# Kernel optimization log

Hardware: AMD Instinct MI355X
Metric: run time of the kernel (lower is better)

## Reference

```python
import jax, jax.numpy as jnp
import numpy as np

DIM = 3072
NUM_HEADS = 24
HEAD_DIM = DIM // NUM_HEADS  # 128
EPS = 1e-6


def rms_norm(x, scale):
    # x: (..., D); torch F.rms_norm over last dim
    var = jnp.mean(jnp.square(x), axis=-1, keepdims=True)
    return x * jax.lax.rsqrt(var + EPS) * scale


def apply_rope(xq, xk, freqs_cis):
    # xq, xk: (B, H, L, D); freqs_cis: (1, 1, L, D//2, 2, 2)
    B, H, L, D = xq.shape
    xq_ = xq.astype(jnp.float32).reshape(B, H, L, D // 2, 1, 2)
    xk_ = xk.astype(jnp.float32).reshape(B, H, L, D // 2, 1, 2)
    # (1,1,L,D/2,2) * (B,H,L,D/2,1) broadcast -> (B,H,L,D/2,2)
    xq_out = freqs_cis[..., 0] * xq_[..., 0] + freqs_cis[..., 1] * xq_[..., 1]
    xk_out = freqs_cis[..., 0] * xk_[..., 0] + freqs_cis[..., 1] * xk_[..., 1]
    return xq_out.reshape(B, H, L, D).astype(xq.dtype), xk_out.reshape(B, H, L, D).astype(xk.dtype)


def setup_inputs() -> dict:
    key = jax.random.key(0)
    ks = jax.random.split(key, 7)
    B, L = 1, 2048
    x = jax.random.normal(ks[0], (B, L, DIM), dtype=jnp.float32)
    pe = jax.random.normal(ks[1], (1, 1, L, HEAD_DIM // 2, 2, 2), dtype=jnp.float32)
    # parameters (torch nn.Linear layout: weight is (out, in))
    s = 1.0 / np.sqrt(DIM)
    w_qkv = jax.random.uniform(ks[2], (3 * DIM, DIM), minval=-s, maxval=s, dtype=jnp.float32)
    w_proj = jax.random.uniform(ks[3], (DIM, DIM), minval=-s, maxval=s, dtype=jnp.float32)
    b_proj = jax.random.uniform(ks[4], (DIM,), minval=-s, maxval=s, dtype=jnp.float32)
    q_scale = jnp.ones((HEAD_DIM,), dtype=jnp.float32)
    k_scale = jnp.ones((HEAD_DIM,), dtype=jnp.float32)
    return {"x": x, "pe": pe, "w_qkv": w_qkv, "w_proj": w_proj,
            "b_proj": b_proj, "q_scale": q_scale, "k_scale": k_scale}


def reference(x, pe, w_qkv, w_proj, b_proj, q_scale, k_scale):
    B, L, _ = x.shape
    qkv = x @ w_qkv.T  # (B, L, 3*DIM)
    qkv = qkv.reshape(B, L, 3, NUM_HEADS, HEAD_DIM)
    qkv = jnp.transpose(qkv, (2, 0, 3, 1, 4))  # (3, B, H, L, D)
    q, k, v = qkv[0], qkv[1], qkv[2]
    # QKNorm (RMSNorm over head_dim)
    q = rms_norm(q, q_scale)
    k = rms_norm(k, k_scale)
    # RoPE
    q, k = apply_rope(q, k, pe)
    # SDPA: softmax(q k^T / sqrt(D)) v, non-causal
    scores = jnp.einsum("bhqd,bhkd->bhqk", q, k) / np.sqrt(HEAD_DIM).astype(np.float32)
    attn = jax.nn.softmax(scores, axis=-1)
    out = jnp.einsum("bhqk,bhkd->bhqd", attn, v)  # (B, H, L, D)
    out = jnp.transpose(out, (0, 2, 1, 3)).reshape(B, L, DIM)  # B L (H D)
    return out @ w_proj.T + b_proj
```

## Files before the change

### kernel.cpp

```cpp
#include <hip/hip_runtime.h>
#include <hip/hip_bf16.h>

typedef _Float16 f16;
typedef _Float16 f16x2 __attribute__((ext_vector_type(2)));
typedef _Float16 f16x4 __attribute__((ext_vector_type(4)));
typedef _Float16 f16x8 __attribute__((ext_vector_type(8)));
typedef float f32x4 __attribute__((ext_vector_type(4)));

#define L_SEQ 2048
#define DIM 3072
#define NHEAD 24
#define HDIM 128

__device__ __forceinline__ void gll16(const f16* g, f16* l) {
    __builtin_amdgcn_global_load_lds((const __attribute__((address_space(1))) void*)g,
                                     (__attribute__((address_space(3))) void*)l, 16, 0, 0);
}

__global__ __launch_bounds__(256) void f32_to_f16_kernel(const float* __restrict__ s,
                                                         f16* __restrict__ d, int n4) {
    int i = blockIdx.x * blockDim.x + threadIdx.x;
    int stride = gridDim.x * blockDim.x;
    for (; i < n4; i += stride) {
        float4 v = reinterpret_cast<const float4*>(s)[i];
        f16x4 o = {(f16)v.x, (f16)v.y, (f16)v.z, (f16)v.w};
        reinterpret_cast<f16x4*>(d)[i] = o;
    }
}


#define PH_BODY(T, VM, DO_STAGE)                                                        \
    {                                                                                   \
        const int slot_ = (T) % 3;                                                      \
        const int s2_ = ((T) + 2) % 3;                                                  \
        const f16* Asl = &As[slot_][0];                                                 \
        const f16* Bsl = &Bs[slot_][0];                                                 \
                        \
        asm volatile("s_waitcnt vmcnt(" #VM ")" ::: "memory");                          \
        __builtin_amdgcn_s_barrier();                                                   \
        __builtin_amdgcn_sched_barrier(0);                                              \
                             \
        f16x8 bf[4][2], af[2][2];                                                       \
        _Pragma("unroll") for (int j = 0; j < 4; j++)                                   \
            _Pragma("unroll") for (int kk = 0; kk < 2; kk++)                            \
                bf[j][kk] = *reinterpret_cast<const f16x8*>(                            \
                    &Bsl[(wc + j * 16 + laneM) * 64 + (((kk << 2) + grp) ^ swz8) * 8]); \
        _Pragma("unroll") for (int u = 0; u < 2; u++)                                   \
            _Pragma("unroll") for (int kk = 0; kk < 2; kk++)                            \
                af[u][kk] = *reinterpret_cast<const f16x8*>(                            \
                    &Asl[(wr + u * 16 + laneM) * 64 + (((kk << 2) + grp) ^ swz8) * 8]); \
        if (DO_STAGE) {                                                                 \
            _Pragma("unroll") for (int i = 0; i < 3; i++)                               \
                gll16(AsrcP + (size_t)(i * 64) * K + ((T) + 2) * 64,                    \
                      &As[s2_][i * 4096 + dstoff]);                                     \
        }                                                                               \
        __builtin_amdgcn_s_barrier();                                                   \
        __builtin_amdgcn_sched_barrier(0);                                              \
        __builtin_amdgcn_s_setprio(1);                                                  \
        _Pragma("unroll") for (int u = 0; u < 2; u++)                                   \
            _Pragma("unroll") for (int j = 0; j < 4; j++)                               \
                _Pragma("unroll") for (int kk = 0; kk < 2; kk++)                        \
                    acc[u][j] = __builtin_amdgcn_mfma_f32_16x16x32_f16(                 \
                        af[u][kk], bf[j][kk], acc[u][j], 0, 0, 0);                      \
        __builtin_amdgcn_s_setprio(0);                                                  \
        __builtin_amdgcn_s_barrier();                                                   \
        __builtin_amdgcn_sched_barrier(0);                                              \
                                             \
        _Pragma("unroll") for (int u = 0; u < 2; u++)                                   \
            _Pragma("unroll") for (int kk = 0; kk < 2; kk++)                            \
                af[u][kk] = *reinterpret_cast<const f16x8*>(                            \
                    &Asl[(wr + 32 + u * 16 + laneM) * 64 +                              \
                         (((kk << 2) + grp) ^ swz8) * 8]);                              \
        if (DO_STAGE) {                                                                 \
            gll16(AsrcP + (size_t)(3 * 64) * K + ((T) + 2) * 64,                        \
                  &As[s2_][3 * 4096 + dstoff]);                                         \
            _Pragma("unroll") for (int i = 0; i < 2; i++)                               \
                gll16(BsrcP + (size_t)(i * 64) * K + ((T) + 2) * 64,                    \
                      &Bs[s2_][i * 4096 + dstoff]);                                     \
        }                                                                               \
        __builtin_amdgcn_s_barrier();                                                   \
        __builtin_amdgcn_sched_barrier(0);                                              \
        __builtin_amdgcn_s_setprio(1);                                                  \
        _Pragma("unroll") for (int u = 0; u < 2; u++)                                   \
            _Pragma("unroll") for (int j = 0; j < 4; j++)                               \
                _Pragma("unroll") for (int kk = 0; kk < 2; kk++)                        \
                    acc[2 + u][j] = __builtin_amdgcn_mfma_f32_16x16x32_f16(             \
                        af[u][kk], bf[j][kk], acc[2 + u][j], 0, 0, 0);                  \
        __builtin_amdgcn_s_setprio(0);                                                  \
    }

template <int MODE>
__global__ __launch_bounds__(512, 2) void ph_gemm(const f16* __restrict__ A,
                                                  const f16* __restrict__ B,
                                                  f16* __restrict__ Cf16,
                                                  float* __restrict__ Cf32,
                                                  const float* __restrict__ bias,
                                                  int M, int N, int K) {
    __shared__ f16 As[3][256 * 64];
    __shared__ f16 Bs[3][128 * 64];
    const int tid = threadIdx.x;
    const int wid = tid >> 6;
    const int lane = tid & 63;
    const int grp = lane >> 4;
    const int laneM = lane & 15;

    const int nwg = gridDim.x * gridDim.y;
    const int orig = blockIdx.y * gridDim.x + blockIdx.x;
    const int wgid = (orig & 7) * (nwg >> 3) + (orig >> 3);
    const int bx = wgid % gridDim.x;
    const int by = wgid / gridDim.x;
    const int m0 = by * 256;
    const int n0 = bx * 128;

    const int wr = (wid >> 1) * 64;
    const int wc = (wid & 1) * 64;
    const int NT = K >> 6;
    const int swz8 = laneM & 7;

    const int sg8 = (((tid & 7) ^ ((tid >> 3) & 7)) << 3);
    const f16* AsrcP = A + (size_t)(m0 + (tid >> 3)) * K + sg8;
    const f16* BsrcP = B + (size_t)(n0 + (tid >> 3)) * K + sg8;
    const int dstoff = wid * 512;

    const f32x4 vzero = {0.f, 0.f, 0.f, 0.f};
    f32x4 acc[4][4];
#pragma unroll
    for (int i = 0; i < 4; i++)
#pragma unroll
        for (int j = 0; j < 4; j++) acc[i][j] = vzero;

#pragma unroll
    for (int t = 0; t < 2; t++) {
#pragma unroll
        for (int i = 0; i < 4; i++)
            gll16(AsrcP + (size_t)(i * 64) * K + t * 64, &As[t][i * 4096 + dstoff]);
#pragma unroll
        for (int i = 0; i < 2; i++)
            gll16(BsrcP + (size_t)(i * 64) * K + t * 64, &Bs[t][i * 4096 + dstoff]);
    }

    int t = 0;
    for (; t < NT - 2; ++t) PH_BODY(t, 6, true);
    PH_BODY(t, 6, false); ++t;
    PH_BODY(t, 0, false);

#pragma unroll
    for (int i = 0; i < 4; i++)
#pragma unroll
        for (int j = 0; j < 4; j++)
#pragma unroll
            for (int r = 0; r < 4; r++) {
                int row = m0 + wr + i * 16 + grp * 4 + r;
                int col = n0 + wc + j * 16 + laneM;
                float v = acc[i][j][r];
                if (MODE == 0) {
                    Cf16[(size_t)row * N + col] = (f16)v;
                } else {
                    Cf32[(size_t)row * N + col] = v + bias[col];
                }
            }
}

__global__ __launch_bounds__(64) void fuse_qk_kernel(const f16* __restrict__ qkv,
                                                     const float* __restrict__ pe,
                                                     const float* __restrict__ qs,
                                                     const float* __restrict__ ks,
                                                     f16* __restrict__ qb,
                                                     f16* __restrict__ kb) {
    const int l = blockIdx.x;
    const int h = blockIdx.y;
    const int i = threadIdx.x;
    const f16* row = qkv + (size_t)l * (3 * DIM) + h * HDIM;
    f16x2 qp = *reinterpret_cast<const f16x2*>(row + 2 * i);
    f16x2 kp = *reinterpret_cast<const f16x2*>(row + DIM + 2 * i);
    float q0 = (float)qp[0], q1 = (float)qp[1];
    float k0 = (float)kp[0], k1 = (float)kp[1];
    float sq = q0 * q0 + q1 * q1;
    float sk = k0 * k0 + k1 * k1;
#pragma unroll
    for (int off = 1; off < 64; off <<= 1) {
        sq += __shfl_xor(sq, off);
        sk += __shfl_xor(sk, off);
    }
    const float SCALE = 0.08838834764831845f;
    float rq = rsqrtf(sq * (1.0f / 128.0f) + 1e-6f) * SCALE;
    float rk = rsqrtf(sk * (1.0f / 128.0f) + 1e-6f);
    float4 w = *reinterpret_cast<const float4*>(pe + ((size_t)l * 64 + i) * 4);
    float qa = q0 * rq * qs[2 * i];
    float qbv = q1 * rq * qs[2 * i + 1];
    float ka = k0 * rk * ks[2 * i];
    float kbv = k1 * rk * ks[2 * i + 1];
    f16x2 qo = {(f16)(w.x * qa + w.y * qbv), (f16)(w.z * qa + w.w * qbv)};
    f16x2 ko = {(f16)(w.x * ka + w.y * kbv), (f16)(w.z * ka + w.w * kbv)};
    *reinterpret_cast<f16x2*>(qb + ((size_t)h * L_SEQ + l) * HDIM + 2 * i) = qo;
    *reinterpret_cast<f16x2*>(kb + ((size_t)h * L_SEQ + l) * HDIM + 2 * i) = ko;
}

__global__ __launch_bounds__(256) void transpose_v_kernel(const f16* __restrict__ qkv,
                                                          f16* __restrict__ vT) {
    __shared__ f16 tile[32][33];
    const int tx = threadIdx.x & 31;
    const int ty = threadIdx.x >> 5;
    const int c0 = blockIdx.x * 32;
    const int r0 = blockIdx.y * 32;
#pragma unroll
    for (int j = 0; j < 4; j++)
        tile[ty + j * 8][tx] = qkv[(size_t)(r0 + ty + j * 8) * (3 * DIM) + 2 * DIM + c0 + tx];
    __syncthreads();
#pragma unroll
    for (int j = 0; j < 4; j++)
        vT[(size_t)(c0 + ty + j * 8) * L_SEQ + r0 + tx] = tile[tx][ty + j * 8];
}

#define KVBLK 64
#define NSTEP (L_SEQ / KVBLK)

__device__ __forceinline__ void stage_kv(const f16* __restrict__ Kh,
                                         const f16* __restrict__ Vh,
                                         int k0, f16* Kt, f16* Vt, int tid) {
    const int wid = tid >> 6;
    const int krow = tid >> 4;
    const int kcl = (tid & 15) ^ (krow & 7);
    const int vrow = tid >> 3;
    const int vcl = (tid & 7) ^ (vrow & 7);
#pragma unroll
    for (int i = 0; i < 4; i++)
        gll16(Kh + (size_t)(k0 + i * 16 + krow) * HDIM + kcl * 8, Kt + i * 2048 + wid * 512);
#pragma unroll
    for (int i = 0; i < 4; i++)
        gll16(Vh + (size_t)(i * 32 + vrow) * L_SEQ + k0 + vcl * 8, Vt + i * 2048 + wid * 512);
}

__global__ __launch_bounds__(256, 2) void attn_kernel(const f16* __restrict__ qb,
                                                      const f16* __restrict__ kb,
                                                      const f16* __restrict__ vT,
                                                      f16* __restrict__ attnb) {
    __shared__ f16 Kt[2][64 * 128];
    __shared__ f16 Vt[2][128 * 64];
    __shared__ f16 Pl[4][16 * 72];
    const int tid = threadIdx.x;
    const int wid = tid >> 6;
    const int lane = tid & 63;
    const int grp = lane >> 4;
    const int laneM = lane & 15;
    const int h = blockIdx.y;
    const int q0 = blockIdx.x * 64 + wid * 16;
    const f16* Qh = qb + (size_t)h * L_SEQ * HDIM;
    const f16* Kh = kb + (size_t)h * L_SEQ * HDIM;
    const f16* Vh = vT + (size_t)h * HDIM * L_SEQ;

    f16x8 qf[4];
#pragma unroll
    for (int c = 0; c < 4; c++)
        qf[c] = *reinterpret_cast<const f16x8*>(Qh + (size_t)(q0 + laneM) * HDIM + c * 32 + grp * 8);

    const f32x4 vzero = {0.f, 0.f, 0.f, 0.f};
    f32x4 O[8];
#pragma unroll
    for (int f = 0; f < 8; f++) O[f] = vzero;
    float m = -3.0e38f;
    float lsum = 0.f;
    f16* Prow = &Pl[wid][laneM * 72];
    const int swz = laneM & 7;

    stage_kv(Kh, Vh, 0, Kt[0], Vt[0], tid);

    for (int step = 0; step < NSTEP; ++step) {
        const int cur = step & 1;
        __syncthreads();
        if (step + 1 < NSTEP)
            stage_kv(Kh, Vh, (step + 1) * KVBLK, Kt[cur ^ 1], Vt[cur ^ 1], tid);
        const f16* Kc = Kt[cur];
        const f16* Vc = Vt[cur];

        f32x4 s[4];
#pragma unroll
        for (int cc = 0; cc < 4; cc++) s[cc] = vzero;
#pragma unroll
        for (int cc = 0; cc < 4; cc++) {
            f16x8 kf[4];
#pragma unroll
            for (int c = 0; c < 4; c++)
                kf[c] = *reinterpret_cast<const f16x8*>(
                    &Kc[(cc * 16 + laneM) * 128 + (((c * 4 + grp) ^ swz) * 8)]);
#pragma unroll
            for (int c = 0; c < 4; c++)
                s[cc] = __builtin_amdgcn_mfma_f32_16x16x32_f16(kf[c], qf[c], s[cc], 0, 0, 0);
        }

        float pmax = s[0][0];
#pragma unroll
        for (int cc = 0; cc < 4; cc++)
#pragma unroll
            for (int r = 0; r < 4; r++) pmax = fmaxf(pmax, s[cc][r]);
        if (!__all(pmax <= m + 8.0f)) {
            float pm = fmaxf(pmax, __shfl_xor(pmax, 16));
            pm = fmaxf(pm, __shfl_xor(pm, 32));
            float mnew = fmaxf(m, pm);
            float alpha = __expf(m - mnew);
            m = mnew;
            lsum *= alpha;
            float af[4];
#pragma unroll
            for (int r = 0; r < 4; r++) af[r] = __shfl(alpha, grp * 4 + r);
#pragma unroll
            for (int f = 0; f < 8; f++)
#pragma unroll
                for (int r = 0; r < 4; r++) O[f][r] *= af[r];
        }
        float ps = 0.f;
#pragma unroll
        for (int cc = 0; cc < 4; cc++) {
            f16x4 pk;
#pragma unroll
            for (int r = 0; r < 4; r++) {
                float p = __expf(s[cc][r] - m);
                ps += p;
                pk[r] = (f16)p;
            }
            *reinterpret_cast<f16x4*>(Prow + cc * 16 + grp * 4) = pk;
        }
        ps += __shfl_xor(ps, 16);
        ps += __shfl_xor(ps, 32);
        lsum += ps;

#pragma unroll
        for (int z = 0; z < 2; z++) {
            f16x8 pa = *reinterpret_cast<const f16x8*>(Prow + z * 32 + grp * 8);
#pragma unroll
            for (int f = 0; f < 8; f++) {
                f16x8 vf = *reinterpret_cast<const f16x8*>(
                    &Vc[(f * 16 + laneM) * 64 + (((z * 4 + grp) ^ swz) * 8)]);
                O[f] = __builtin_amdgcn_mfma_f32_16x16x32_f16(pa, vf, O[f], 0, 0, 0);
            }
        }
    }

    float li = 1.0f / lsum;
    float lf[4];
#pragma unroll
    for (int r = 0; r < 4; r++) lf[r] = __shfl(li, grp * 4 + r);
#pragma unroll
    for (int f = 0; f < 8; f++)
#pragma unroll
        for (int r = 0; r < 4; r++) {
            int row = q0 + grp * 4 + r;
            attnb[(size_t)row * DIM + h * HDIM + f * 16 + laneM] = (f16)(O[f][r] * lf[r]);
        }
}

extern "C" void kernel_launch(void* const* d_in, const int* in_sizes, int n_in,
                              void* d_out, int out_size, void* d_ws, size_t ws_size,
                              hipStream_t stream) {
    const float* x = (const float*)d_in[0];
    const float* pe = (const float*)d_in[1];
    const float* w_qkv = (const float*)d_in[2];
    const float* w_proj = (const float*)d_in[3];
    const float* b_proj = (const float*)d_in[4];
    const float* q_scale = (const float*)d_in[5];
    const float* k_scale = (const float*)d_in[6];
    float* out = (float*)d_out;

    char* ws = (char*)d_ws;
    f16* xb     = (f16*)(ws + 0);
    f16* wqkvb  = (f16*)(ws + 12582912);
    f16* wprojb = (f16*)(ws + 69206016);
    f16* qkvb   = (f16*)(ws + 88080384);
    f16* qbuf   = (f16*)(ws + 125829120);
    f16* kbuf   = (f16*)(ws + 138412032);
    f16* vT     = (f16*)(ws + 150994944);
    f16* attnb  = (f16*)(ws + 163577856);
    if (ws_size < 176160768) return;

    f32_to_f16_kernel<<<1024, 256, 0, stream>>>(x, xb, (2048 * 3072) / 4);
    f32_to_f16_kernel<<<2048, 256, 0, stream>>>(w_qkv, wqkvb, (9216 * 3072) / 4);
    f32_to_f16_kernel<<<1024, 256, 0, stream>>>(w_proj, wprojb, (3072 * 3072) / 4);

    ph_gemm<0><<<dim3(72, 8), 512, 0, stream>>>(xb, wqkvb, qkvb, nullptr, nullptr,
                                                2048, 9216, 3072);
    fuse_qk_kernel<<<dim3(2048, 24), 64, 0, stream>>>(qkvb, pe, q_scale, k_scale, qbuf, kbuf);
    transpose_v_kernel<<<dim3(96, 64), 256, 0, stream>>>(qkvb, vT);
    attn_kernel<<<dim3(32, 24), 256, 0, stream>>>(qbuf, kbuf, vT, attnb);
    ph_gemm<1><<<dim3(24, 8), 512, 0, stream>>>(attnb, wprojb, nullptr, out, b_proj,
                                                2048, 3072, 3072);
}
```

Before: 377.1 us.

## Add dedicated QKV GEMM writing transposed V directly, drop transpose kernel

```diff
diff --git a/kernel.cpp b/kernel.cpp
--- a/kernel.cpp
+++ b/kernel.cpp
@@ -29,17 +29,124 @@
 }
 
 
+#define GEMM_BODY_S(T, VM, DO_STAGE)                                                    \
+    {                                                                                   \
+        asm volatile("s_waitcnt vmcnt(" #VM ")" ::: "memory");                          \
+        __builtin_amdgcn_s_barrier();                                                   \
+        __builtin_amdgcn_sched_barrier(0);                                              \
+        const int slot_ = (T) % 3;                                                      \
+        f16x8 af[4], bf[4];                                                             \
+        _Pragma("unroll") for (int i = 0; i < 4; i++)                                   \
+            af[i] = *reinterpret_cast<const f16x8*>(                                    \
+                &As[slot_][(wr + i * 16 + laneM) * 32 + fc16]);                         \
+        _Pragma("unroll") for (int j = 0; j < 4; j++)                                   \
+            bf[j] = *reinterpret_cast<const f16x8*>(                                    \
+                &Bs[slot_][(wc + j * 16 + laneM) * 32 + fc16]);                         \
+        if (DO_STAGE) {                                                                 \
+            const int t2 = (T) + 2;                                                     \
+            const int s2 = t2 % 3;                                                      \
+            gll16(Asrc + t2 * 32, &As[s2][dstoff]);                                     \
+            gll16(Asrc + (size_t)64 * K + t2 * 32, &As[s2][2048 + dstoff]);             \
+            gll16(Bsrc + t2 * 32, &Bs[s2][dstoff]);                                     \
+            gll16(Bsrc + (size_t)64 * K + t2 * 32, &Bs[s2][2048 + dstoff]);             \
+        }                                                                               \
+        __builtin_amdgcn_s_setprio(1);                                                  \
+        _Pragma("unroll") for (int i = 0; i < 4; i++)                                   \
+            _Pragma("unroll") for (int j = 0; j < 4; j++)                               \
+                acc[i][j] =                                                             \
+                    __builtin_amdgcn_mfma_f32_16x16x32_f16(af[i], bf[j], acc[i][j],     \
+                                                           0, 0, 0);                    \
+        __builtin_amdgcn_s_setprio(0);                                                  \
+    }
+
+__global__ __launch_bounds__(256, 4) void qkv_gemm(const f16* __restrict__ A,
+                                                   const f16* __restrict__ B,
+                                                   f16* __restrict__ Cf16,
+                                                   f16* __restrict__ vT,
+                                                   int M, int N, int K) {
+    __shared__ f16 As[3][128 * 32];
+    __shared__ f16 Bs[3][128 * 32];
+    const int tid = threadIdx.x;
+    const int wid = tid >> 6;
+    const int lane = tid & 63;
+    const int grp = lane >> 4;
+    const int laneM = lane & 15;
+
+    const int nwg = gridDim.x * gridDim.y;
+    const int orig = blockIdx.y * gridDim.x + blockIdx.x;
+    const int wgid = (orig & 7) * (nwg >> 3) + (orig >> 3);
+    const int by = wgid % gridDim.y;
+    const int bx = wgid / gridDim.y;
+    const int m0 = by * 128;
+    const int n0 = bx * 128;
+
+    const int wr = (wid >> 1) * 64;
+    const int wc = (wid & 1) * 64;
+    const int NT = K >> 5;
+    const int fc16 = (grp ^ ((laneM >> 1) & 3)) * 8;
+
+    const int srow = tid >> 2;
+    const int scol = (((tid & 3) ^ ((tid >> 3) & 3)) << 3);
+    const f16* Asrc = A + (size_t)(m0 + srow) * K + scol;
+    const f16* Bsrc = B + (size_t)(n0 + srow) * K + scol;
+    const int dstoff = wid * 512;
+
+    const f32x4 vzero = {0.f, 0.f, 0.f, 0.f};
+    f32x4 acc[4][4];
+#pragma unroll
+    for (int i = 0; i < 4; i++)
+#pragma unroll
+        for (int j = 0; j < 4; j++) acc[i][j] = vzero;
+
+#pragma unroll
+    for (int t = 0; t < 2; t++) {
+        gll16(Asrc + t * 32, &As[t][dstoff]);
+        gll16(Asrc + (size_t)64 * K + t * 32, &As[t][2048 + dstoff]);
+        gll16(Bsrc + t * 32, &Bs[t][dstoff]);
+        gll16(Bsrc + (size_t)64 * K + t * 32, &Bs[t][2048 + dstoff]);
+    }
+
+    int t = 0;
+    for (; t < NT - 2; ++t) GEMM_BODY_S(t, 4, true);
+    GEMM_BODY_S(t, 4, false); ++t;
+    GEMM_BODY_S(t, 0, false);
+
+    if (n0 < 2 * DIM) {
+#pragma unroll
+        for (int i = 0; i < 4; i++)
+#pragma unroll
+            for (int j = 0; j < 4; j++)
+#pragma unroll
+                for (int r = 0; r < 4; r++) {
+                    int row = m0 + wr + i * 16 + grp * 4 + r;
+                    int col = n0 + wc + j * 16 + laneM;
+                    Cf16[(size_t)row * N + col] = (f16)acc[i][j][r];
+                }
+    } else {
+#pragma unroll
+        for (int i = 0; i < 4; i++)
+#pragma unroll
+            for (int j = 0; j < 4; j++) {
+                int hd = n0 - 2 * DIM + wc + j * 16 + laneM;
+                int row0 = m0 + wr + i * 16 + grp * 4;
+                f16x4 pk;
+#pragma unroll
+                for (int r = 0; r < 4; r++) pk[r] = (f16)acc[i][j][r];
+                *reinterpret_cast<f16x4*>(&vT[(size_t)hd * L_SEQ + row0]) = pk;
+            }
+    }
+}
+
+
 #define PH_BODY(T, VM, DO_STAGE)                                                        \
     {                                                                                   \
         const int slot_ = (T) % 3;                                                      \
         const int s2_ = ((T) + 2) % 3;                                                  \
         const f16* Asl = &As[slot_][0];                                                 \
         const f16* Bsl = &Bs[slot_][0];                                                 \
-                        \
         asm volatile("s_waitcnt vmcnt(" #VM ")" ::: "memory");                          \
         __builtin_amdgcn_s_barrier();                                                   \
         __builtin_amdgcn_sched_barrier(0);                                              \
-                             \
         f16x8 bf[4][2], af[2][2];                                                       \
         _Pragma("unroll") for (int j = 0; j < 4; j++)                                   \
             _Pragma("unroll") for (int kk = 0; kk < 2; kk++)                            \
@@ -65,7 +172,6 @@
         __builtin_amdgcn_s_setprio(0);                                                  \
         __builtin_amdgcn_s_barrier();                                                   \
         __builtin_amdgcn_sched_barrier(0);                                              \
-                                             \
         _Pragma("unroll") for (int u = 0; u < 2; u++)                                   \
             _Pragma("unroll") for (int kk = 0; kk < 2; kk++)                            \
                 af[u][kk] = *reinterpret_cast<const f16x8*>(                            \
@@ -89,13 +195,11 @@
         __builtin_amdgcn_s_setprio(0);                                                  \
     }
 
-template <int MODE>
-__global__ __launch_bounds__(512, 2) void ph_gemm(const f16* __restrict__ A,
-                                                  const f16* __restrict__ B,
-                                                  f16* __restrict__ Cf16,
-                                                  float* __restrict__ Cf32,
-                                                  const float* __restrict__ bias,
-                                                  int M, int N, int K) {
+__global__ __launch_bounds__(512, 2) void proj_gemm(const f16* __restrict__ A,
+                                                    const f16* __restrict__ B,
+                                                    float* __restrict__ Cf32,
+                                                    const float* __restrict__ bias,
+                                                    int M, int N, int K) {
     __shared__ f16 As[3][256 * 64];
     __shared__ f16 Bs[3][128 * 64];
     const int tid = threadIdx.x;
@@ -152,24 +256,19 @@
             for (int r = 0; r < 4; r++) {
                 int row = m0 + wr + i * 16 + grp * 4 + r;
                 int col = n0 + wc + j * 16 + laneM;
-                float v = acc[i][j][r];
-                if (MODE == 0) {
-                    Cf16[(size_t)row * N + col] = (f16)v;
-                } else {
-                    Cf32[(size_t)row * N + col] = v + bias[col];
-                }
+                Cf32[(size_t)row * N + col] = acc[i][j][r] + bias[col];
             }
 }
 
-__global__ __launch_bounds__(64) void fuse_qk_kernel(const f16* __restrict__ qkv,
-                                                     const float* __restrict__ pe,
-                                                     const float* __restrict__ qs,
-                                                     const float* __restrict__ ks,
-                                                     f16* __restrict__ qb,
-                                                     f16* __restrict__ kb) {
+__global__ __launch_bounds__(256) void fuse_qk_kernel(const f16* __restrict__ qkv,
+                                                      const float* __restrict__ pe,
+                                                      const float* __restrict__ qs,
+                                                      const float* __restrict__ ks,
+                                                      f16* __restrict__ qb,
+                                                      f16* __restrict__ kb) {
     const int l = blockIdx.x;
-    const int h = blockIdx.y;
-    const int i = threadIdx.x;
+    const int h = blockIdx.y * 4 + (threadIdx.x >> 6);
+    const int i = threadIdx.x & 63;
     const f16* row = qkv + (size_t)l * (3 * DIM) + h * HDIM;
     f16x2 qp = *reinterpret_cast<const f16x2*>(row + 2 * i);
     f16x2 kp = *reinterpret_cast<const f16x2*>(row + DIM + 2 * i);
@@ -194,22 +293,6 @@
     f16x2 ko = {(f16)(w.x * ka + w.y * kbv), (f16)(w.z * ka + w.w * kbv)};
     *reinterpret_cast<f16x2*>(qb + ((size_t)h * L_SEQ + l) * HDIM + 2 * i) = qo;
     *reinterpret_cast<f16x2*>(kb + ((size_t)h * L_SEQ + l) * HDIM + 2 * i) = ko;
-}
-
-__global__ __launch_bounds__(256) void transpose_v_kernel(const f16* __restrict__ qkv,
-                                                          f16* __restrict__ vT) {
-    __shared__ f16 tile[32][33];
-    const int tx = threadIdx.x & 31;
-    const int ty = threadIdx.x >> 5;
-    const int c0 = blockIdx.x * 32;
-    const int r0 = blockIdx.y * 32;
-#pragma unroll
-    for (int j = 0; j < 4; j++)
-        tile[ty + j * 8][tx] = qkv[(size_t)(r0 + ty + j * 8) * (3 * DIM) + 2 * DIM + c0 + tx];
-    __syncthreads();
-#pragma unroll
-    for (int j = 0; j < 4; j++)
-        vT[(size_t)(c0 + ty + j * 8) * L_SEQ + r0 + tx] = tile[tx][ty + j * 8];
 }
 
 #define KVBLK 64
@@ -376,11 +459,8 @@
     f32_to_f16_kernel<<<2048, 256, 0, stream>>>(w_qkv, wqkvb, (9216 * 3072) / 4);
     f32_to_f16_kernel<<<1024, 256, 0, stream>>>(w_proj, wprojb, (3072 * 3072) / 4);
 
-    ph_gemm<0><<<dim3(72, 8), 512, 0, stream>>>(xb, wqkvb, qkvb, nullptr, nullptr,
-                                                2048, 9216, 3072);
-    fuse_qk_kernel<<<dim3(2048, 24), 64, 0, stream>>>(qkvb, pe, q_scale, k_scale, qbuf, kbuf);
-    transpose_v_kernel<<<dim3(96, 64), 256, 0, stream>>>(qkvb, vT);
+    qkv_gemm<<<dim3(72, 16), 256, 0, stream>>>(xb, wqkvb, qkvb, vT, 2048, 9216, 3072);
+    fuse_qk_kernel<<<dim3(2048, 6), 256, 0, stream>>>(qkvb, pe, q_scale, k_scale, qbuf, kbuf);
     attn_kernel<<<dim3(32, 24), 256, 0, stream>>>(qbuf, kbuf, vT, attnb);
-    ph_gemm<1><<<dim3(24, 8), 512, 0, stream>>>(attnb, wprojb, nullptr, out, b_proj,
-                                                2048, 3072, 3072);
-}
+    proj_gemm<<<dim3(24, 8), 512, 0, stream>>>(attnb, wprojb, out, b_proj, 2048, 3072, 3072);
+}
```

New measurement: 365.3 us. -3.1%, faster.
